# Performance work log

Hardware: AMD Instinct MI355X
Metric: run time of the kernel (lower is better)

## Reference

```python
import jax, jax.numpy as jnp
import numpy as np

B, T, S, E, H = 2, 2048, 2048, 1024, 16
DH = E // H

def setup_inputs() -> dict:
    key = jax.random.key(0)
    ks = jax.random.split(key, 12)
    sc = 1.0 / np.sqrt(E)
    inp = {
        'query': jax.random.normal(ks[0], (B, T, E), jnp.float32),
        'key':   jax.random.normal(ks[1], (B, S, E), jnp.float32),
        'value': jax.random.normal(ks[2], (B, S, E), jnp.float32),
        'Wq': jax.random.normal(ks[3], (E, E), jnp.float32) * sc,
        'bq': jnp.zeros((E,), jnp.float32),
        'Wk': jax.random.normal(ks[4], (E, E), jnp.float32) * sc,
        'bk': jnp.zeros((E,), jnp.float32),
        'Wv': jax.random.normal(ks[5], (E, E), jnp.float32) * sc,
        'bv': jnp.zeros((E,), jnp.float32),
        'Wo': jax.random.normal(ks[6], (E, E), jnp.float32) * sc,
        'bo': jnp.zeros((E,), jnp.float32),
    }
    return inp

def reference(query, key, value, Wq, bq, Wk, bk, Wv, bv, Wo, bo):
    # Linear projections (torch nn.Linear: x @ W.T + b)
    Q = query @ Wq.T + bq          # [B,T,E]
    K = key   @ Wk.T + bk          # [B,S,E]
    V = value @ Wv.T + bv          # [B,S,E]
    # split heads -> [B,H,L,DH]
    Q = Q.reshape(B, T, H, DH).transpose(0, 2, 1, 3)
    K = K.reshape(B, S, H, DH).transpose(0, 2, 1, 3)
    V = V.reshape(B, S, H, DH).transpose(0, 2, 1, 3)
    scores = jnp.einsum('bhtd,bhsd->bhts', Q, K) / jnp.sqrt(jnp.float32(DH))
    attn = jax.nn.softmax(scores, axis=-1)            # [B,H,T,S]
    out = jnp.einsum('bhts,bhsd->bhtd', attn, V)      # [B,H,T,DH]
    out = out.transpose(0, 2, 1, 3).reshape(B, T, E)
    out = out @ Wo.T + bo                             # [B,T,E]
    attn_avg = attn.mean(axis=1)                      # average_attn_weights=True
    return out, attn_avg
```

## Files before the change

kernel.cpp:

```cpp
#include <hip/hip_runtime.h>

#define DEV __device__ __forceinline__

typedef __attribute__((ext_vector_type(8))) short short8;
typedef __attribute__((ext_vector_type(4))) float floatx4;
typedef __attribute__((ext_vector_type(2))) unsigned int uint2v;
typedef unsigned short u16;

DEV u16 f2bf(float f) {
  unsigned int u = __float_as_uint(f);
  u += 0x7fffu + ((u >> 16) & 1u);
  return (u16)(u >> 16);
}

DEV unsigned int cvtpk(float a, float b) {
  unsigned int r;
  asm("v_cvt_pk_bf16_f32 %0, %1, %2" : "=v"(r) : "v"(a), "v"(b));
  return r;
}

DEV void load16_to_lds(const void* g, void* l) {
  __builtin_amdgcn_global_load_lds(
      (const __attribute__((address_space(1))) unsigned int*)g,
      (__attribute__((address_space(3))) unsigned int*)l, 16, 0, 0);
}

DEV int xcd_swz(int flat, int nwg) {
  return (flat & 7) * (nwg >> 3) + (flat >> 3);
}

#define MFMA16(A, B, C) __builtin_amdgcn_mfma_f32_16x16x32_bf16(A, B, C, 0, 0, 0)
#define EXP2(x) __builtin_amdgcn_exp2f(x)

#define QSCALE 0.18033688011112042f

DEV void stage_block(const u16* src_row0, int k0, int ln, void* ldsbase) {
  int r = ln >> 2;
  int p = ((ln & 3) - (ln >> 4)) & 3;
  load16_to_lds((const char*)(src_row0 + (size_t)r * 1024 + k0) + p * 16, ldsbase);
}
DEV const short8* frag_addr(const u16* base, int blk, int c, int q) {
  int slot = c * 4 + ((q + (c >> 2)) & 3);
  return (const short8*)(base + blk * 512 + slot * 8);
}

__global__ __launch_bounds__(256) void cvt_all(
    const float* __restrict__ w0, const float* __restrict__ w1,
    const float* __restrict__ w2, const float* __restrict__ w3,
    const float* __restrict__ a0, const float* __restrict__ a1, const float* __restrict__ a2,
    u16* __restrict__ e0, u16* __restrict__ e1, u16* __restrict__ e2, u16* __restrict__ e3,
    u16* __restrict__ f0, u16* __restrict__ f1, u16* __restrict__ f2) {
  const int t = blockIdx.y;
  const float* s;
  u16* d;
  size_t base;
  if (t < 4) {
    s = t == 0 ? w0 : t == 1 ? w1 : t == 2 ? w2 : w3;
    d = t == 0 ? e0 : t == 1 ? e1 : t == 2 ? e2 : e3;
    base = 0;
  } else {
    int a = (t - 4) >> 2;
    s = a == 0 ? a0 : a == 1 ? a1 : a2;
    d = a == 0 ? f0 : a == 1 ? f1 : f2;
    base = (size_t)((t - 4) & 3) * 1048576;
  }
  size_t i = base + (size_t)(blockIdx.x * 256 + threadIdx.x) * 4;
  float4 v = *(const float4*)(s + i);
  ushort4 o;
  o.x = f2bf(v.x); o.y = f2bf(v.y); o.z = f2bf(v.z); o.w = f2bf(v.w);
  *(ushort4*)(d + i) = o;
}

__global__ __launch_bounds__(512, 4) void qkv_gemm(
    const u16* __restrict__ qb, const u16* __restrict__ kb, const u16* __restrict__ vb,
    const u16* __restrict__ wq, const u16* __restrict__ wk, const u16* __restrict__ wv,
    const float* __restrict__ bq, const float* __restrict__ bk, const float* __restrict__ bv,
    u16* __restrict__ Qh, u16* __restrict__ Kh, u16* __restrict__ VT) {
  __shared__ __align__(16) u16 As[2][8192];
  __shared__ __align__(16) u16 Bs[2][4096];
  const int tid = threadIdx.x;
  const int w = tid >> 6, ln = tid & 63, q = ln >> 4, c = ln & 15;
  const int wr = w >> 1, wc = w & 1;
  const int z = blockIdx.z;
  int m_idx, n_idx;
  if (z == 2) {
    int f2 = blockIdx.x + 8 * blockIdx.y;
    n_idx = f2 & 31;
    m_idx = f2 >> 5;
  } else {
    n_idx = blockIdx.x;
    m_idx = blockIdx.y;
  }
  const int m0 = m_idx * 256, n0 = n_idx * 128;
  const u16* Asrc = z == 0 ? qb : (z == 1 ? kb : wv);
  const u16* Bsrc = z == 0 ? wq : (z == 1 ? wk : vb);

  floatx4 acc[4][4];
#pragma unroll
  for (int i = 0; i < 4; ++i)
#pragma unroll
    for (int j = 0; j < 4; ++j) acc[i][j] = (floatx4){0.f, 0.f, 0.f, 0.f};

#pragma unroll
  for (int j = 0; j < 3; ++j) {
    int idx = w * 3 + j;
    if (idx < 16)
      stage_block(Asrc + (size_t)(m0 + idx * 16) * 1024, 0, ln, (char*)As[0] + idx * 1024);
    else
      stage_block(Bsrc + (size_t)(n0 + (idx - 16) * 16) * 1024, 0, ln, (char*)Bs[0] + (idx - 16) * 1024);
  }

  int cur = 0;
  for (int k0 = 0; k0 < 1024; k0 += 32) {
    __syncthreads();
    if (k0 + 32 < 1024) {
      const int nb = cur ^ 1;
#pragma unroll
      for (int j = 0; j < 3; ++j) {
        int idx = w * 3 + j;
        if (idx < 16)
          stage_block(Asrc + (size_t)(m0 + idx * 16) * 1024, k0 + 32, ln, (char*)As[nb] + idx * 1024);
        else
          stage_block(Bsrc + (size_t)(n0 + (idx - 16) * 16) * 1024, k0 + 32, ln,
                      (char*)Bs[nb] + (idx - 16) * 1024);
      }
    }
    short8 a[4], bb[4];
#pragma unroll
    for (int mt = 0; mt < 4; ++mt) a[mt] = *frag_addr(As[cur], wr * 4 + mt, c, q);
#pragma unroll
    for (int nt = 0; nt < 4; ++nt) bb[nt] = *frag_addr(Bs[cur], wc * 4 + nt, c, q);
    __builtin_amdgcn_s_setprio(1);
#pragma unroll
    for (int mt = 0; mt < 4; ++mt)
#pragma unroll
      for (int nt = 0; nt < 4; ++nt) acc[mt][nt] = MFMA16(a[mt], bb[nt], acc[mt][nt]);
    __builtin_amdgcn_s_setprio(0);
    cur ^= 1;
  }

  if (z <= 1) {
    const float* bias = z ? bk : bq;
    u16* dst = z ? Kh : Qh;
    const float scale = z ? 1.0f : QSCALE;
    float bn[4];
#pragma unroll
    for (int nt = 0; nt < 4; ++nt) bn[nt] = bias[n0 + wc * 64 + nt * 16 + c];
#pragma unroll
    for (int mt = 0; mt < 4; ++mt)
#pragma unroll
      for (int r = 0; r < 4; ++r) {
        int m = m0 + wr * 64 + mt * 16 + 4 * q + r;
        int bbv = m >> 11, t = m & 2047;
#pragma unroll
        for (int nt = 0; nt < 4; ++nt) {
          int n = n0 + wc * 64 + nt * 16 + c;
          dst[((size_t)(bbv * 16 + (n >> 6)) * 2048 + t) * 64 + (n & 63)] =
              f2bf((acc[mt][nt][r] + bn[nt]) * scale);
        }
      }
  } else {
    float bm[4][4];
#pragma unroll
    for (int mt = 0; mt < 4; ++mt)
#pragma unroll
      for (int r = 0; r < 4; ++r) bm[mt][r] = bv[m0 + wr * 64 + mt * 16 + 4 * q + r];
#pragma unroll
    for (int mt = 0; mt < 4; ++mt)
#pragma unroll
      for (int r = 0; r < 4; ++r) {
        int d = m0 + wr * 64 + mt * 16 + 4 * q + r;
        int hh = d >> 6, dl = d & 63;
#pragma unroll
        for (int nt = 0; nt < 4; ++nt) {
          int s = n0 + wc * 64 + nt * 16 + c;
          int bbv = s >> 11, sl = s & 2047;
          VT[((size_t)(bbv * 16 + hh) * 64 + dl) * 2048 + sl] = f2bf(acc[mt][nt][r] + bm[mt][r]);
        }
      }
  }
}

__global__ __launch_bounds__(256) void oproj_gemm(const u16* __restrict__ Ap, const u16* __restrict__ Wp,
                                                  const float* __restrict__ bias, float* __restrict__ out) {
  __shared__ __align__(16) u16 As[2][4096];
  __shared__ __align__(16) u16 Bs[2][4096];
  const int tid = threadIdx.x;
  const int w = tid >> 6, ln = tid & 63, q = ln >> 4, c = ln & 15;
  const int wr = w >> 1, wc = w & 1;
  const int n0 = blockIdx.x * 128, m0 = blockIdx.y * 128;

  floatx4 acc[4][4];
#pragma unroll
  for (int i = 0; i < 4; ++i)
#pragma unroll
    for (int j = 0; j < 4; ++j) acc[i][j] = (floatx4){0.f, 0.f, 0.f, 0.f};

#pragma unroll
  for (int it = 0; it < 2; ++it) {
    int I = w * 2 + it;
    stage_block(Ap + (size_t)(m0 + I * 16) * 1024, 0, ln, (char*)As[0] + I * 1024);
    stage_block(Wp + (size_t)(n0 + I * 16) * 1024, 0, ln, (char*)Bs[0] + I * 1024);
  }

  int cur = 0;
  for (int k0 = 0; k0 < 1024; k0 += 32) {
    __syncthreads();
    if (k0 + 32 < 1024) {
      const int nb = cur ^ 1;
#pragma unroll
      for (int it = 0; it < 2; ++it) {
        int I = w * 2 + it;
        stage_block(Ap + (size_t)(m0 + I * 16) * 1024, k0 + 32, ln, (char*)As[nb] + I * 1024);
        stage_block(Wp + (size_t)(n0 + I * 16) * 1024, k0 + 32, ln, (char*)Bs[nb] + I * 1024);
      }
    }
    short8 a[4], bb[4];
#pragma unroll
    for (int mt = 0; mt < 4; ++mt) a[mt] = *frag_addr(As[cur], wr * 4 + mt, c, q);
#pragma unroll
    for (int nt = 0; nt < 4; ++nt) bb[nt] = *frag_addr(Bs[cur], wc * 4 + nt, c, q);
    __builtin_amdgcn_s_setprio(1);
#pragma unroll
    for (int mt = 0; mt < 4; ++mt)
#pragma unroll
      for (int nt = 0; nt < 4; ++nt) acc[mt][nt] = MFMA16(a[mt], bb[nt], acc[mt][nt]);
    __builtin_amdgcn_s_setprio(0);
    cur ^= 1;
  }

  float bn[4];
#pragma unroll
  for (int nt = 0; nt < 4; ++nt) bn[nt] = bias[n0 + wc * 64 + nt * 16 + c];
#pragma unroll
  for (int mt = 0; mt < 4; ++mt)
#pragma unroll
    for (int r = 0; r < 4; ++r) {
      int m = m0 + wr * 64 + mt * 16 + 4 * q + r;
#pragma unroll
      for (int nt = 0; nt < 4; ++nt)
        out[(size_t)m * 1024 + n0 + wc * 64 + nt * 16 + c] = acc[mt][nt][r] + bn[nt];
    }
}

__global__ __launch_bounds__(512, 4) void flash_attn(const u16* __restrict__ Qh, const u16* __restrict__ Kh,
                                                     const u16* __restrict__ VhT, u16* __restrict__ Obuf,
                                                     float* __restrict__ l_ws) {
  __shared__ __align__(16) u16 Ks[2][4096];
  __shared__ __align__(16) u16 VTs[3][4096];
  __shared__ __align__(16) u16 Ps[8][2][1152];
  const int tid = threadIdx.x;
  const int w = tid >> 6, ln = tid & 63, q = ln >> 4, c = ln & 15;
  const int lg = xcd_swz(blockIdx.x + 16 * (blockIdx.y + 16 * blockIdx.z), 512);
  const int t0 = (lg & 15) * 128, h = (lg >> 4) & 15, b = lg >> 8;
  const size_t bh = (size_t)(b * 16 + h);
  const u16* Qbase = Qh + bh * 131072;
  const u16* Kbase = Kh + bh * 131072;
  const u16* Vbase = VhT + bh * 131072;

  short8 qf0, qf1;
  {
    const u16* qr = Qbase + (size_t)(t0 + w * 16 + c) * 64 + q * 8;
    qf0 = *(const short8*)qr;
    qf1 = *(const short8*)(qr + 32);
  }
  floatx4 oacc[4];
  float lacc = 0.f;
#pragma unroll
  for (int j = 0; j < 4; ++j) oacc[j] = (floatx4){0.f, 0.f, 0.f, 0.f};

  const int srow = ln >> 3;
  const int sch = (ln & 7) ^ srow;
  const int cx = c & 7;
  const int row = w * 8 + srow;

  load16_to_lds((const char*)Kbase + ((size_t)row * 64 + sch * 8) * 2, (char*)Ks[0] + w * 1024);
  load16_to_lds((const char*)Vbase + ((size_t)row * 2048 + sch * 8) * 2, (char*)VTs[0] + w * 1024);

  int vc = 0;
  for (int i = 0; i < 32; ++i) {
    const int s0 = i * 64;
    __syncthreads();
    int vn = vc + 1;
    if (vn == 3) vn = 0;
    int vp = vc - 1;
    if (vp < 0) vp = 2;
    if (i + 1 < 32) {
      load16_to_lds((const char*)Kbase + ((size_t)(s0 + 64 + row) * 64 + sch * 8) * 2,
                    (char*)Ks[(i + 1) & 1] + w * 1024);
      load16_to_lds((const char*)Vbase + ((size_t)row * 2048 + (s0 + 64) + sch * 8) * 2,
                    (char*)VTs[vn] + w * 1024);
    }
    const u16* ks = Ks[i & 1];
    floatx4 zz[4];
    __builtin_amdgcn_s_setprio(1);
#pragma unroll
    for (int st = 0; st < 4; ++st) {
      const int rr = st * 16 + c;
      short8 k0 = *(const short8*)(ks + rr * 64 + ((q ^ cx) << 3));
      short8 k1 = *(const short8*)(ks + rr * 64 + (((4 + q) ^ cx) << 3));
      zz[st] = (floatx4){0.f, 0.f, 0.f, 0.f};
      zz[st] = MFMA16(k0, qf0, zz[st]);
      zz[st] = MFMA16(k1, qf1, zz[st]);
    }
    __builtin_amdgcn_s_setprio(0);
    if (i > 0) {
      const u16* vs = VTs[vp];
      const u16* pw = Ps[w][(i - 1) & 1];
      short8 pf0 = *(const short8*)(pw + c * 72 + q * 8);
      short8 pf1 = *(const short8*)(pw + c * 72 + 32 + q * 8);
      __builtin_amdgcn_s_setprio(1);
#pragma unroll
      for (int dt = 0; dt < 4; ++dt) {
        const int rr = dt * 16 + c;
        short8 v0 = *(const short8*)(vs + rr * 64 + ((q ^ cx) << 3));
        short8 v1 = *(const short8*)(vs + rr * 64 + (((4 + q) ^ cx) << 3));
        oacc[dt] = MFMA16(pf0, v0, oacc[dt]);
        oacc[dt] = MFMA16(pf1, v1, oacc[dt]);
      }
      __builtin_amdgcn_s_setprio(0);
    }
    u16* pwr = Ps[w][i & 1];
#pragma unroll
    for (int st = 0; st < 4; ++st) {
      float e0 = EXP2(zz[st][0]), e1 = EXP2(zz[st][1]), e2 = EXP2(zz[st][2]), e3 = EXP2(zz[st][3]);
      lacc += (e0 + e1) + (e2 + e3);
      uint2v pk = {cvtpk(e0, e1), cvtpk(e2, e3)};
      *(uint2v*)(pwr + c * 72 + st * 16 + 4 * q) = pk;
    }
    vc = vn;
  }
  {
    const u16* vs = VTs[1];
    const u16* pw = Ps[w][1];
    short8 pf0 = *(const short8*)(pw + c * 72 + q * 8);
    short8 pf1 = *(const short8*)(pw + c * 72 + 32 + q * 8);
#pragma unroll
    for (int dt = 0; dt < 4; ++dt) {
      const int rr = dt * 16 + c;
      short8 v0 = *(const short8*)(vs + rr * 64 + ((q ^ cx) << 3));
      short8 v1 = *(const short8*)(vs + rr * 64 + (((4 + q) ^ cx) << 3));
      oacc[dt] = MFMA16(pf0, v0, oacc[dt]);
      oacc[dt] = MFMA16(pf1, v1, oacc[dt]);
    }
  }
  {
    float v = lacc;
    v += __shfl_xor(v, 16);
    v += __shfl_xor(v, 32);
    lacc = v;
    if (q == 0) l_ws[bh * 2048 + t0 + w * 16 + c] = v;
  }
#pragma unroll
  for (int r = 0; r < 4; ++r) {
    float lv = __shfl(lacc, 4 * q + r);
    float inv = __builtin_amdgcn_rcpf(lv);
    const int t = t0 + w * 16 + 4 * q + r;
#pragma unroll
    for (int dt = 0; dt < 4; ++dt)
      Obuf[((size_t)b * 2048 + t) * 1024 + h * 64 + dt * 16 + c] = f2bf(oacc[dt][r] * inv);
  }
}

__global__ __launch_bounds__(256) void attn_avg_k(const u16* __restrict__ Qh, const u16* __restrict__ Kh,
                                                  const float* __restrict__ l_ws, float* __restrict__ out2) {
  __shared__ __align__(16) u16 Ks[2][4096];
  const int tid = threadIdx.x;
  const int w = tid >> 6, ln = tid & 63, q = ln >> 4, c = ln & 15;
  const int lg = xcd_swz(blockIdx.x + 32 * (blockIdx.y + 16 * blockIdx.z), 1024);
  const int s0 = (lg & 31) * 64, t0 = ((lg >> 5) & 15) * 128, b = lg >> 9;
  const int srow = ln >> 3;
  const int sch = (ln & 7) ^ srow;
  const int cx = c & 7;

  floatx4 acc[2][4];
#pragma unroll
  for (int i = 0; i < 2; ++i)
#pragma unroll
    for (int j = 0; j < 4; ++j) acc[i][j] = (floatx4){0.f, 0.f, 0.f, 0.f};

#pragma unroll
  for (int it = 0; it < 2; ++it) {
    int I = w * 2 + it;
    int row = I * 8 + srow;
    load16_to_lds((const char*)(Kh + (size_t)(b * 16) * 131072) + ((size_t)(s0 + row) * 64 + sch * 8) * 2,
                  (char*)Ks[0] + I * 1024);
  }

  for (int h = 0; h < 16; ++h) {
    const size_t bh = (size_t)(b * 16 + h);
    const u16* ks = Ks[h & 1];
    __syncthreads();
    if (h < 15) {
      const u16* Kn = Kh + (bh + 1) * 131072;
#pragma unroll
      for (int it = 0; it < 2; ++it) {
        int I = w * 2 + it;
        int row = I * 8 + srow;
        load16_to_lds((const char*)Kn + ((size_t)(s0 + row) * 64 + sch * 8) * 2,
                      (char*)Ks[(h + 1) & 1] + I * 1024);
      }
    }
    short8 qf[2][2];
    float linv[2];
#pragma unroll
    for (int blk = 0; blk < 2; ++blk) {
      const u16* qr = Qh + bh * 131072 + (size_t)(t0 + w * 32 + blk * 16 + c) * 64 + q * 8;
      qf[blk][0] = *(const short8*)qr;
      qf[blk][1] = *(const short8*)(qr + 32);
      linv[blk] = __builtin_amdgcn_rcpf(l_ws[bh * 2048 + t0 + w * 32 + blk * 16 + c]) * 0.0625f;
    }
#pragma unroll
    for (int st = 0; st < 4; ++st) {
      const int row = st * 16 + c;
      short8 k0 = *(const short8*)(ks + row * 64 + ((q ^ cx) << 3));
      short8 k1 = *(const short8*)(ks + row * 64 + (((4 + q) ^ cx) << 3));
#pragma unroll
      for (int blk = 0; blk < 2; ++blk) {
        floatx4 zz = (floatx4){0.f, 0.f, 0.f, 0.f};
        zz = MFMA16(k0, qf[blk][0], zz);
        zz = MFMA16(k1, qf[blk][1], zz);
#pragma unroll
        for (int r = 0; r < 4; ++r) acc[blk][st][r] += EXP2(zz[r]) * linv[blk];
      }
    }
  }
#pragma unroll
  for (int blk = 0; blk < 2; ++blk) {
    const size_t t = (size_t)t0 + w * 32 + blk * 16 + c;
#pragma unroll
    for (int st = 0; st < 4; ++st) {
      float4 o;
      o.x = acc[blk][st][0]; o.y = acc[blk][st][1]; o.z = acc[blk][st][2]; o.w = acc[blk][st][3];
      *(float4*)(out2 + ((size_t)b * 2048 + t) * 2048 + s0 + st * 16 + 4 * q) = o;
    }
  }
}

extern "C" void kernel_launch(void* const* d_in, const int* in_sizes, int n_in,
                              void* d_out, int out_size, void* d_ws, size_t ws_size,
                              hipStream_t stream) {
  const float* query = (const float*)d_in[0];
  const float* key = (const float*)d_in[1];
  const float* value = (const float*)d_in[2];
  const float* Wq = (const float*)d_in[3];
  const float* bq = (const float*)d_in[4];
  const float* Wk = (const float*)d_in[5];
  const float* bk = (const float*)d_in[6];
  const float* Wv = (const float*)d_in[7];
  const float* bv = (const float*)d_in[8];
  const float* Wo = (const float*)d_in[9];
  const float* bo = (const float*)d_in[10];

  char* ws = (char*)d_ws;
  const size_t MB = 1024 * 1024;
  u16* wWq = (u16*)(ws + 0 * MB);
  u16* wWk = (u16*)(ws + 2 * MB);
  u16* wWv = (u16*)(ws + 4 * MB);
  u16* wWo = (u16*)(ws + 6 * MB);
  u16* wQh = (u16*)(ws + 8 * MB);
  u16* wKh = (u16*)(ws + 16 * MB);
  u16* wVT = (u16*)(ws + 24 * MB);
  u16* wO = (u16*)(ws + 32 * MB);
  float* wl = (float*)(ws + 40 * MB);
  float* out = (float*)d_out;
  float* out2 = out + (size_t)4194304;

  u16* qb = (u16*)out2;
  u16* kb = qb + 4194304;
  u16* vb = kb + 4194304;

  cvt_all<<<dim3(1024, 16), 256, 0, stream>>>(Wq, Wk, Wv, Wo, query, key, value,
                                              wWq, wWk, wWv, wWo, qb, kb, vb);
  qkv_gemm<<<dim3(8, 16, 3), 512, 0, stream>>>(qb, kb, vb, wWq, wWk, wWv,
                                               bq, bk, bv, wQh, wKh, wVT);
  flash_attn<<<dim3(16, 16, 2), 512, 0, stream>>>(wQh, wKh, wVT, wO, wl);
  attn_avg_k<<<dim3(32, 16, 2), 256, 0, stream>>>(wQh, wKh, wl, out2);
  oproj_gemm<<<dim3(8, 32), 256, 0, stream>>>(wO, wWo, bo, out);
}
```

Before: 266.7 us.

## Retile QKV GEMM to 128x128 tiles with 4 waves and K-step 64

The QKV projection GEMM now uses 256-thread blocks (4 waves, 2x2) on 128x128 output tiles instead of 512 threads on 256x128. Each pipeline stage loads a K-chunk of 64 as two 32-wide halves, which halves the number of barriers per tile. The grid grows to 8x32x3, and the swizzled block index mapping for the transposed V projection is replaced by a plain swap of x and y. The intent is fewer synchronizations and better load balance across CUs, at the cost of more LDS per block and less operand reuse per tile.

```diff
diff --git a/kernel.cpp b/kernel.cpp
--- a/kernel.cpp
+++ b/kernel.cpp
@@ -71,27 +71,19 @@
   *(ushort4*)(d + i) = o;
 }
 
-__global__ __launch_bounds__(512, 4) void qkv_gemm(
+__global__ __launch_bounds__(256) void qkv_gemm(
     const u16* __restrict__ qb, const u16* __restrict__ kb, const u16* __restrict__ vb,
     const u16* __restrict__ wq, const u16* __restrict__ wk, const u16* __restrict__ wv,
     const float* __restrict__ bq, const float* __restrict__ bk, const float* __restrict__ bv,
     u16* __restrict__ Qh, u16* __restrict__ Kh, u16* __restrict__ VT) {
   __shared__ __align__(16) u16 As[2][8192];
-  __shared__ __align__(16) u16 Bs[2][4096];
+  __shared__ __align__(16) u16 Bs[2][8192];
   const int tid = threadIdx.x;
   const int w = tid >> 6, ln = tid & 63, q = ln >> 4, c = ln & 15;
   const int wr = w >> 1, wc = w & 1;
   const int z = blockIdx.z;
-  int m_idx, n_idx;
-  if (z == 2) {
-    int f2 = blockIdx.x + 8 * blockIdx.y;
-    n_idx = f2 & 31;
-    m_idx = f2 >> 5;
-  } else {
-    n_idx = blockIdx.x;
-    m_idx = blockIdx.y;
-  }
-  const int m0 = m_idx * 256, n0 = n_idx * 128;
+  const int m0 = (z == 2 ? blockIdx.x : blockIdx.y) * 128;
+  const int n0 = (z == 2 ? blockIdx.y : blockIdx.x) * 128;
   const u16* Asrc = z == 0 ? qb : (z == 1 ? kb : wv);
   const u16* Bsrc = z == 0 ? wq : (z == 1 ? wk : vb);
 
@@ -102,40 +94,50 @@
     for (int j = 0; j < 4; ++j) acc[i][j] = (floatx4){0.f, 0.f, 0.f, 0.f};
 
 #pragma unroll
-  for (int j = 0; j < 3; ++j) {
-    int idx = w * 3 + j;
+  for (int j = 0; j < 8; ++j) {
+    int idx = w * 8 + j;
+    int rb = idx & 7, h2 = (idx >> 3) & 1;
     if (idx < 16)
-      stage_block(Asrc + (size_t)(m0 + idx * 16) * 1024, 0, ln, (char*)As[0] + idx * 1024);
+      stage_block(Asrc + (size_t)(m0 + rb * 16) * 1024, h2 * 32, ln,
+                  (char*)As[0] + h2 * 8192 + rb * 1024);
     else
-      stage_block(Bsrc + (size_t)(n0 + (idx - 16) * 16) * 1024, 0, ln, (char*)Bs[0] + (idx - 16) * 1024);
+      stage_block(Bsrc + (size_t)(n0 + rb * 16) * 1024, h2 * 32, ln,
+                  (char*)Bs[0] + h2 * 8192 + rb * 1024);
   }
 
   int cur = 0;
-  for (int k0 = 0; k0 < 1024; k0 += 32) {
+  for (int k0 = 0; k0 < 1024; k0 += 64) {
     __syncthreads();
-    if (k0 + 32 < 1024) {
+    if (k0 + 64 < 1024) {
       const int nb = cur ^ 1;
 #pragma unroll
-      for (int j = 0; j < 3; ++j) {
-        int idx = w * 3 + j;
+      for (int j = 0; j < 8; ++j) {
+        int idx = w * 8 + j;
+        int rb = idx & 7, h2 = (idx >> 3) & 1;
         if (idx < 16)
-          stage_block(Asrc + (size_t)(m0 + idx * 16) * 1024, k0 + 32, ln, (char*)As[nb] + idx * 1024);
+          stage_block(Asrc + (size_t)(m0 + rb * 16) * 1024, k0 + 64 + h2 * 32, ln,
+                      (char*)As[nb] + h2 * 8192 + rb * 1024);
         else
-          stage_block(Bsrc + (size_t)(n0 + (idx - 16) * 16) * 1024, k0 + 32, ln,
-                      (char*)Bs[nb] + (idx - 16) * 1024);
-      }
-    }
-    short8 a[4], bb[4];
-#pragma unroll
-    for (int mt = 0; mt < 4; ++mt) a[mt] = *frag_addr(As[cur], wr * 4 + mt, c, q);
-#pragma unroll
-    for (int nt = 0; nt < 4; ++nt) bb[nt] = *frag_addr(Bs[cur], wc * 4 + nt, c, q);
-    __builtin_amdgcn_s_setprio(1);
-#pragma unroll
-    for (int mt = 0; mt < 4; ++mt)
-#pragma unroll
-      for (int nt = 0; nt < 4; ++nt) acc[mt][nt] = MFMA16(a[mt], bb[nt], acc[mt][nt]);
-    __builtin_amdgcn_s_setprio(0);
+          stage_block(Bsrc + (size_t)(n0 + rb * 16) * 1024, k0 + 64 + h2 * 32, ln,
+                      (char*)Bs[nb] + h2 * 8192 + rb * 1024);
+      }
+    }
+#pragma unroll
+    for (int h2 = 0; h2 < 2; ++h2) {
+      const u16* Ab = As[cur] + h2 * 4096;
+      const u16* Bb = Bs[cur] + h2 * 4096;
+      short8 a[4], bb[4];
+#pragma unroll
+      for (int mt = 0; mt < 4; ++mt) a[mt] = *frag_addr(Ab, wr * 4 + mt, c, q);
+#pragma unroll
+      for (int nt = 0; nt < 4; ++nt) bb[nt] = *frag_addr(Bb, wc * 4 + nt, c, q);
+      __builtin_amdgcn_s_setprio(1);
+#pragma unroll
+      for (int mt = 0; mt < 4; ++mt)
+#pragma unroll
+        for (int nt = 0; nt < 4; ++nt) acc[mt][nt] = MFMA16(a[mt], bb[nt], acc[mt][nt]);
+      __builtin_amdgcn_s_setprio(0);
+    }
     cur ^= 1;
   }
 
@@ -472,7 +474,7 @@
 
   cvt_all<<<dim3(1024, 16), 256, 0, stream>>>(Wq, Wk, Wv, Wo, query, key, value,
                                               wWq, wWk, wWv, wWo, qb, kb, vb);
-  qkv_gemm<<<dim3(8, 16, 3), 512, 0, stream>>>(qb, kb, vb, wWq, wWk, wWv,
+  qkv_gemm<<<dim3(8, 32, 3), 256, 0, stream>>>(qb, kb, vb, wWq, wWk, wWv,
                                                bq, bk, bv, wQh, wKh, wVT);
   flash_attn<<<dim3(16, 16, 2), 512, 0, stream>>>(wQh, wKh, wVT, wO, wl);
   attn_avg_k<<<dim3(32, 16, 2), 256, 0, stream>>>(wQh, wKh, wl, out2);
```

Result: slower. 277.6 us (+4.1%).
